# Optimization experiments

Hardware: AMD Instinct MI355X
Metric: run time of the kernel (lower is better)

## Reference

```python
import jax, jax.numpy as jnp
import numpy as np

N_NODES = 8192
EMBED = 64
N_NEURONS = [512, 256, 128]
ACTION_SIZE = 8
BATCH = 4096


def setup_inputs() -> dict:
    key = jax.random.key(0)
    ks = jax.random.split(key, 16)
    in_size = 2 * N_NODES + 2 * EMBED

    def u(k, shape, bound):
        return jax.random.uniform(k, shape, jnp.float32, -bound, bound)

    stdv1 = 1.0 / np.sqrt(N_NEURONS[0])
    stdv2 = 1.0 / np.sqrt(EMBED)
    return {
        "state": jax.random.uniform(ks[0], (N_NODES, N_NODES), jnp.float32),
        "start": jax.random.randint(ks[1], (BATCH,), 0, N_NODES),
        "end": jax.random.randint(ks[2], (BATCH,), 0, N_NODES),
        # GCN layer params
        "gw1": u(ks[3], (1, N_NEURONS[0]), stdv1),
        "gb1": u(ks[4], (N_NEURONS[0],), stdv1),
        "gw2": u(ks[5], (N_NEURONS[0], EMBED), stdv2),
        "gb2": u(ks[6], (EMBED,), stdv2),
        # dense head params (xavier-ish)
        "fw1": u(ks[7], (in_size, N_NEURONS[0]), np.sqrt(6.0 / (in_size + N_NEURONS[0]))),
        "fb1": jnp.zeros((N_NEURONS[0],), jnp.float32),
        "fw2": u(ks[8], (N_NEURONS[0], N_NEURONS[1]), np.sqrt(6.0 / (N_NEURONS[0] + N_NEURONS[1]))),
        "fb2": jnp.zeros((N_NEURONS[1],), jnp.float32),
        "fw3": u(ks[9], (N_NEURONS[1], N_NEURONS[2]), np.sqrt(6.0 / (N_NEURONS[1] + N_NEURONS[2]))),
        "fb3": jnp.zeros((N_NEURONS[2],), jnp.float32),
        "fw4": u(ks[10], (N_NEURONS[2], ACTION_SIZE), np.sqrt(6.0 / (N_NEURONS[2] + ACTION_SIZE))),
        "fb4": jnp.zeros((ACTION_SIZE,), jnp.float32),
    }


def reference(state, start, end, gw1, gb1, gw2, gb2,
              fw1, fb1, fw2, fb2, fw3, fb3, fw4, fb4):
    # x = diag(state) as [N, 1] node features
    x = jnp.diagonal(state)[:, None]
    # adj = state with zeroed diagonal, detached (no grad through adj)
    adj = jax.lax.stop_gradient(jnp.fill_diagonal(state, 0.0, inplace=False))
    # GCN layer 1: relu(adj @ (x @ W) + b); dropout is identity in eval mode
    h = jax.nn.relu(adj @ (x @ gw1) + gb1)              # [N, 512]
    # GCN layer 2
    h = jax.nn.relu(adj @ (h @ gw2) + gb2)              # [N, 64]
    h = jax.nn.log_softmax(h, axis=1)                   # [N, 64]
    # gather node features and embeddings for each (start, end) edge
    edge_features = jnp.concatenate(
        [state[start], state[end], h[start], h[end]], axis=1)  # [B, 2N+2E]
    y = jax.nn.relu(edge_features @ fw1 + fb1)
    y = jax.nn.relu(y @ fw2 + fb2)                      # d1 dropout: identity (eval)
    y = jax.nn.relu(y @ fw3 + fb3)
    action_q = jax.nn.relu(y @ fw4 + fb4)               # [B, action_size]
    return action_q
```

## Files before the change

### kernel.cpp

```cpp
#include <hip/hip_runtime.h>
#include <hip/hip_bf16.h>
#include <math.h>

#define NN 8192
#define EMB 64
#define H1D 512
#define NB 4096

typedef __bf16 bf16x8 __attribute__((ext_vector_type(8)));
typedef float f32x4 __attribute__((ext_vector_type(4)));
typedef unsigned short u16x8 __attribute__((ext_vector_type(8)));
typedef unsigned short u16x4 __attribute__((ext_vector_type(4)));

__device__ __forceinline__ unsigned short f2bf(float f) {
    return __bfloat16_as_ushort(__float2bfloat16(f));
}

__device__ __forceinline__ void gload16(const void* g, void* l) {
    __builtin_amdgcn_global_load_lds(
        (const __attribute__((address_space(1))) void*)g,
        (__attribute__((address_space(3))) void*)l, 16, 0, 0);
}

__global__ void k_diag(const float* __restrict__ state, float* __restrict__ diag) {
    int i = blockIdx.x * blockDim.x + threadIdx.x;
    if (i < NN) diag[i] = state[(size_t)i * NN + i];
}

__global__ __launch_bounds__(256) void k_convert(const float* __restrict__ state,
                                                 const float* __restrict__ diag,
                                                 unsigned short* __restrict__ stateb,
                                                 float* __restrict__ s) {
    int row = blockIdx.x;
    int tid = threadIdx.x;
    const float4* st4 = (const float4*)(state + (size_t)row * NN);
    const float4* dg4 = (const float4*)diag;
    unsigned short* drow = stateb + (size_t)row * NN;
    float acc = 0.f;
#pragma unroll
    for (int t = 0; t < 8; ++t) {
        int f = t * 256 + tid;
        float4 a = st4[f], d = dg4[f];
        acc += a.x * d.x + a.y * d.y + a.z * d.z + a.w * d.w;
        u16x4 o;
        o[0] = f2bf(a.x); o[1] = f2bf(a.y); o[2] = f2bf(a.z); o[3] = f2bf(a.w);
        *(u16x4*)&drow[f * 4] = o;
    }
#pragma unroll
    for (int m = 32; m >= 1; m >>= 1) acc += __shfl_xor(acc, m);
    __shared__ float red[4];
    if ((tid & 63) == 0) red[tid >> 6] = acc;
    __syncthreads();
    if (tid == 0) {
        float tot = red[0] + red[1] + red[2] + red[3];
        float d = diag[row];
        s[row] = tot - d * d;
    }
}

__global__ __launch_bounds__(256) void k_tr_fw1(const float* __restrict__ fw1,
                                                unsigned short* __restrict__ fw1t) {
    __shared__ float t[64][65];
    int kb = blockIdx.x * 64, nb = blockIdx.y * 64;
    int tid = threadIdx.x;
#pragma unroll
    for (int i = 0; i < 4; ++i) {
        int lin = i * 256 + tid;
        int r = lin >> 4, c4 = (lin & 15) << 2;
        float4 v = *(const float4*)&fw1[(size_t)(kb + r) * 512 + nb + c4];
        t[r][c4] = v.x; t[r][c4 + 1] = v.y; t[r][c4 + 2] = v.z; t[r][c4 + 3] = v.w;
    }
    __syncthreads();
#pragma unroll
    for (int i = 0; i < 4; ++i) {
        int lin = i * 256 + tid;
        int n = lin >> 4, k4 = (lin & 15) << 2;
        u16x4 o;
        o[0] = f2bf(t[k4 + 0][n]); o[1] = f2bf(t[k4 + 1][n]);
        o[2] = f2bf(t[k4 + 2][n]); o[3] = f2bf(t[k4 + 3][n]);
        *(u16x4*)&fw1t[(size_t)(nb + n) * 16512 + kb + k4] = o;
    }
}

__global__ __launch_bounds__(256) void k_tr_w(const float* __restrict__ W,
                                              unsigned short* __restrict__ Wt,
                                              int K, int N) {
    __shared__ float t[64][65];
    int kb = blockIdx.x * 64, nb = blockIdx.y * 64;
    int tid = threadIdx.x;
#pragma unroll
    for (int i = 0; i < 4; ++i) {
        int lin = i * 256 + tid;
        int r = lin >> 4, c4 = (lin & 15) << 2;
        float4 v = *(const float4*)&W[(size_t)(kb + r) * N + nb + c4];
        t[r][c4] = v.x; t[r][c4 + 1] = v.y; t[r][c4 + 2] = v.z; t[r][c4 + 3] = v.w;
    }
    __syncthreads();
#pragma unroll
    for (int i = 0; i < 4; ++i) {
        int lin = i * 256 + tid;
        int n = lin >> 4, k4 = (lin & 15) << 2;
        u16x4 o;
        o[0] = f2bf(t[k4 + 0][n]); o[1] = f2bf(t[k4 + 1][n]);
        o[2] = f2bf(t[k4 + 2][n]); o[3] = f2bf(t[k4 + 3][n]);
        *(u16x4*)&Wt[(size_t)(nb + n) * K + kb + k4] = o;
    }
}

__global__ __launch_bounds__(256) void k_tr_q(const float* __restrict__ q,
                                              unsigned short* __restrict__ qbT) {
    __shared__ float t[64][65];
    int kb = blockIdx.x * 64;
    int tid = threadIdx.x;
#pragma unroll
    for (int i = 0; i < 4; ++i) {
        int lin = i * 256 + tid;
        int r = lin >> 4, c4 = (lin & 15) << 2;
        float4 v = *(const float4*)&q[(size_t)(kb + r) * 64 + c4];
        t[r][c4] = v.x; t[r][c4 + 1] = v.y; t[r][c4 + 2] = v.z; t[r][c4 + 3] = v.w;
    }
    __syncthreads();
#pragma unroll
    for (int i = 0; i < 4; ++i) {
        int lin = i * 256 + tid;
        int c = lin >> 4, k4 = (lin & 15) << 2;
        u16x4 o;
        o[0] = f2bf(t[k4 + 0][c]); o[1] = f2bf(t[k4 + 1][c]);
        o[2] = f2bf(t[k4 + 2][c]); o[3] = f2bf(t[k4 + 3][c]);
        *(u16x4*)&qbT[(size_t)c * 8192 + kb + k4] = o;
    }
}

__global__ __launch_bounds__(256) void k_rowdot(const float* __restrict__ state,
                                                const float* __restrict__ diag,
                                                float* __restrict__ s) {
    int row = blockIdx.x;
    int tid = threadIdx.x;
    const float4* st4 = (const float4*)(state + (size_t)row * NN);
    const float4* dg4 = (const float4*)diag;
    float acc = 0.f;
#pragma unroll
    for (int t = 0; t < 8; ++t) {
        int f = t * 256 + tid;
        float4 a = st4[f], d = dg4[f];
        acc += a.x * d.x + a.y * d.y + a.z * d.z + a.w * d.w;
    }
#pragma unroll
    for (int m = 32; m >= 1; m >>= 1) acc += __shfl_xor(acc, m);
    __shared__ float red[4];
    if ((tid & 63) == 0) red[tid >> 6] = acc;
    __syncthreads();
    if (tid == 0) {
        float tot = red[0] + red[1] + red[2] + red[3];
        float d = diag[row];
        s[row] = tot - d * d;
    }
}

__global__ __launch_bounds__(256) void k_q(const float* __restrict__ s,
                                           const float* __restrict__ gw1,
                                           const float* __restrict__ gb1,
                                           const float* __restrict__ gw2,
                                           float* __restrict__ q) {
    __shared__ float sg1[H1D], sb1[H1D];
    int tid = threadIdx.x;
    for (int i = tid; i < H1D; i += 256) { sg1[i] = gw1[i]; sb1[i] = gb1[i]; }
    __syncthreads();
    int c = tid & 63;
    int row = blockIdx.x * 4 + (tid >> 6);
    float sv = s[row];
    float a0 = 0.f, a1 = 0.f, a2 = 0.f, a3 = 0.f;
    for (int j = 0; j < H1D; j += 4) {
        float h0 = fmaxf(fmaf(sv, sg1[j + 0], sb1[j + 0]), 0.f);
        float h1 = fmaxf(fmaf(sv, sg1[j + 1], sb1[j + 1]), 0.f);
        float h2 = fmaxf(fmaf(sv, sg1[j + 2], sb1[j + 2]), 0.f);
        float h3 = fmaxf(fmaf(sv, sg1[j + 3], sb1[j + 3]), 0.f);
        a0 = fmaf(h0, gw2[(j + 0) * EMB + c], a0);
        a1 = fmaf(h1, gw2[(j + 1) * EMB + c], a1);
        a2 = fmaf(h2, gw2[(j + 2) * EMB + c], a2);
        a3 = fmaf(h3, gw2[(j + 3) * EMB + c], a3);
    }
    q[row * EMB + c] = (a0 + a1) + (a2 + a3);
}


__global__ __launch_bounds__(256) void k_gcn2_mfma_b(const unsigned short* __restrict__ stateb,
                                                     const unsigned short* __restrict__ qbT,
                                                     float* __restrict__ partg) {
    __shared__ __align__(16) unsigned short Asm[2][64 * 64];
    __shared__ __align__(16) unsigned short Bsm[2][64 * 64];
    const int tid = threadIdx.x;
    const int l = tid & 63, wv = tid >> 6;
    const int rbase = blockIdx.x * 64;
    const int kbase0 = blockIdx.y * 1024;

    const unsigned short* aP[2]; const unsigned short* bP[2]; int lb[2];
#pragma unroll
    for (int i = 0; i < 2; ++i) {
        int slot = i * 256 + tid;
        int r = slot >> 3, cg = slot & 7;
        aP[i] = stateb + (size_t)(rbase + r) * NN + kbase0 + ((cg ^ (r & 7)) << 3);
        bP[i] = qbT + (size_t)r * 8192 + kbase0 + ((cg ^ (r & 7)) << 3);
        lb[i] = slot * 8;
    }

    f32x4 acc[4] = {};
    const int fr = l & 15, fq = l >> 4;

#pragma unroll
    for (int i = 0; i < 2; ++i) {
        gload16(aP[i], &Asm[0][lb[i]]);
        gload16(bP[i], &Bsm[0][lb[i]]);
    }
    __syncthreads();

    int buf = 0;
    for (int kt = 0; kt < 16; ++kt) {
        if (kt < 15) {
#pragma unroll
            for (int i = 0; i < 2; ++i) {
                gload16(aP[i] + (kt + 1) * 64, &Asm[buf ^ 1][lb[i]]);
                gload16(bP[i] + (kt + 1) * 64, &Bsm[buf ^ 1][lb[i]]);
            }
        }
#pragma unroll
        for (int kh = 0; kh < 2; ++kh) {
            int ch = kh * 4 + fq;
            int row = wv * 16 + fr;
            bf16x8 aF = *(const bf16x8*)&Asm[buf][row * 64 + ((ch ^ (row & 7)) << 3)];
            bf16x8 bF[4];
#pragma unroll
            for (int n = 0; n < 4; ++n) {
                int col = n * 16 + fr;
                bF[n] = *(const bf16x8*)&Bsm[buf][col * 64 + ((ch ^ (col & 7)) << 3)];
            }
#pragma unroll
            for (int n = 0; n < 4; ++n)
                acc[n] = __builtin_amdgcn_mfma_f32_16x16x32_bf16(aF, bF[n], acc[n], 0, 0, 0);
        }
        __syncthreads();
        buf ^= 1;
    }

    float* dst = partg + (size_t)blockIdx.y * (NN * EMB);
#pragma unroll
    for (int n = 0; n < 4; ++n) {
        int row0 = rbase + wv * 16 + fq * 4;
        int col = n * 16 + fr;
#pragma unroll
        for (int j = 0; j < 4; ++j)
            dst[(size_t)(row0 + j) * EMB + col] = acc[n][j];
    }
}

__global__ __launch_bounds__(256) void k_gcn2_combine_b(const float* __restrict__ partg,
                                                        const float* __restrict__ diag,
                                                        const float* __restrict__ q,
                                                        const float* __restrict__ gb2,
                                                        unsigned short* __restrict__ hb) {
    int tid = threadIdx.x;
    int c = tid & 63;
    int row = blockIdx.x * 4 + (tid >> 6);
    int idx = row * EMB + c;
    float v = gb2[c] - diag[row] * q[idx];
#pragma unroll
    for (int p = 0; p < 8; ++p) v += partg[(size_t)p * NN * EMB + idx];
    v = fmaxf(v, 0.f);
    float mx = v;
#pragma unroll
    for (int m = 32; m >= 1; m >>= 1) mx = fmaxf(mx, __shfl_xor(mx, m));
    float e = expf(v - mx);
    float sum = e;
#pragma unroll
    for (int m = 32; m >= 1; m >>= 1) sum += __shfl_xor(sum, m);
    hb[idx] = f2bf(v - mx - logf(sum));
}

__global__ __launch_bounds__(256) void k_head1_mfma_b(
    const unsigned short* __restrict__ stateb, const unsigned short* __restrict__ hb,
    const int* __restrict__ start, const int* __restrict__ end,
    const unsigned short* __restrict__ fw1t, float* __restrict__ parth) {
    __shared__ __align__(16) unsigned short Asm[128 * 64];
    __shared__ __align__(16) unsigned short Bsm[128 * 64];
    __shared__ int ridx[128];
    const int tid = threadIdx.x;
    const int l = tid & 63, wv = tid >> 6;
    const int rbase = blockIdx.x * 128, cbase = blockIdx.y * 128;
    const int ks = blockIdx.z, side = ks >> 1, half = ks & 1;
    if (tid < 128) ridx[tid] = (side ? end : start)[rbase + tid];
    __syncthreads();

    const unsigned short* aS[4]; const unsigned short* aH[4];
    const unsigned short* bP[4];
    unsigned short* aL[4]; unsigned short* bL[4];
#pragma unroll
    for (int i = 0; i < 4; ++i) {
        int slot = i * 256 + tid;
        int r = slot >> 3, cg = slot & 7;
        int swz = (cg ^ (r & 7)) << 3;
        int gi = ridx[r];
        aS[i] = stateb + (size_t)gi * NN + half * 4096 + swz;
        aH[i] = hb + gi * EMB + swz;
        bP[i] = fw1t + (size_t)(cbase + r) * 16512 + swz;
        aL[i] = &Asm[slot * 8];
        bL[i] = &Bsm[slot * 8];
    }
    const int kB0 = side * 8192 + half * 4096;
    const int kBtail = 16384 + side * 64;
    const int nsteps = 64 + half;

    f32x4 acc[4][4] = {};
    const int wm = wv >> 1, wn = wv & 1;
    const int fr = l & 15, fq = l >> 4;

    for (int kt = 0; kt < nsteps; ++kt) {
        if (kt < 64) {
#pragma unroll
            for (int i = 0; i < 4; ++i) {
                gload16(aS[i] + kt * 64, aL[i]);
                gload16(bP[i] + kB0 + kt * 64, bL[i]);
            }
        } else {
#pragma unroll
            for (int i = 0; i < 4; ++i) {
                gload16(aH[i], aL[i]);
                gload16(bP[i] + kBtail, bL[i]);
            }
        }
        __syncthreads();
#pragma unroll
        for (int kh = 0; kh < 2; ++kh) {
            int ch = kh * 4 + fq;
            bf16x8 aF[4], bF[4];
#pragma unroll
            for (int m = 0; m < 4; ++m) {
                int row = wm * 64 + m * 16 + fr;
                aF[m] = *(const bf16x8*)&Asm[row * 64 + ((ch ^ (row & 7)) << 3)];
            }
#pragma unroll
            for (int n = 0; n < 4; ++n) {
                int nl = wn * 64 + n * 16 + fr;
                bF[n] = *(const bf16x8*)&Bsm[nl * 64 + ((ch ^ (nl & 7)) << 3)];
            }
#pragma unroll
            for (int m = 0; m < 4; ++m)
#pragma unroll
                for (int n = 0; n < 4; ++n)
                    acc[m][n] = __builtin_amdgcn_mfma_f32_16x16x32_bf16(
                        aF[m], bF[n], acc[m][n], 0, 0, 0);
        }
        __syncthreads();
    }

    float* dst = parth + (size_t)ks * (NB * H1D);
#pragma unroll
    for (int m = 0; m < 4; ++m) {
        int row0 = rbase + wm * 64 + m * 16 + fq * 4;
#pragma unroll
        for (int n = 0; n < 4; ++n) {
            int col = cbase + wn * 64 + n * 16 + fr;
#pragma unroll
            for (int j = 0; j < 4; ++j)
                dst[(size_t)(row0 + j) * H1D + col] = acc[m][n][j];
        }
    }
}

__global__ void k_head1_fin4(const float* __restrict__ parth, const float* __restrict__ fb1,
                             unsigned short* __restrict__ y1b) {
    int i = blockIdx.x * blockDim.x + threadIdx.x;
    const size_t S = (size_t)NB * H1D;
    float4 a = *(const float4*)&parth[(size_t)i * 4];
    float4 b = *(const float4*)&parth[S + (size_t)i * 4];
    float4 c = *(const float4*)&parth[2 * S + (size_t)i * 4];
    float4 d = *(const float4*)&parth[3 * S + (size_t)i * 4];
    float4 bias = *(const float4*)&fb1[(i * 4) & 511];
    u16x4 o;
    o[0] = f2bf(fmaxf(a.x + b.x + c.x + d.x + bias.x, 0.f));
    o[1] = f2bf(fmaxf(a.y + b.y + c.y + d.y + bias.y, 0.f));
    o[2] = f2bf(fmaxf(a.z + b.z + c.z + d.z + bias.z, 0.f));
    o[3] = f2bf(fmaxf(a.w + b.w + c.w + d.w + bias.w, 0.f));
    *(u16x4*)&y1b[(size_t)i * 4] = o;
}

__global__ __launch_bounds__(256) void k_ff1(const unsigned short* __restrict__ A,
                                             const unsigned short* __restrict__ Wt,
                                             const float* __restrict__ bias,
                                             unsigned short* __restrict__ out) {
    __shared__ __align__(16) unsigned short Asm[128 * 64];
    __shared__ __align__(16) unsigned short Bsm[128 * 64];
    const int tid = threadIdx.x;
    const int l = tid & 63, wv = tid >> 6;
    const int rbase = blockIdx.x * 128, cbase = blockIdx.y * 128;

    const unsigned short* aP[4]; const unsigned short* bP[4];
    unsigned short* aL[4]; unsigned short* bL[4];
#pragma unroll
    for (int i = 0; i < 4; ++i) {
        int slot = i * 256 + tid;
        int r = slot >> 3, cg = slot & 7;
        int swz = (cg ^ (r & 7)) << 3;
        aP[i] = A + (size_t)(rbase + r) * 512 + swz;
        bP[i] = Wt + (size_t)(cbase + r) * 512 + swz;
        aL[i] = &Asm[slot * 8];
        bL[i] = &Bsm[slot * 8];
    }

    f32x4 acc[4][4] = {};
    const int wm = wv >> 1, wn = wv & 1;
    const int fr = l & 15, fq = l >> 4;

    for (int kt = 0; kt < 8; ++kt) {
#pragma unroll
        for (int i = 0; i < 4; ++i) {
            gload16(aP[i] + kt * 64, aL[i]);
            gload16(bP[i] + kt * 64, bL[i]);
        }
        __syncthreads();
#pragma unroll
        for (int kh = 0; kh < 2; ++kh) {
            int ch = kh * 4 + fq;
            bf16x8 aF[4], bF[4];
#pragma unroll
            for (int m = 0; m < 4; ++m) {
                int row = wm * 64 + m * 16 + fr;
                aF[m] = *(const bf16x8*)&Asm[row * 64 + ((ch ^ (row & 7)) << 3)];
            }
#pragma unroll
            for (int n = 0; n < 4; ++n) {
                int nl = wn * 64 + n * 16 + fr;
                bF[n] = *(const bf16x8*)&Bsm[nl * 64 + ((ch ^ (nl & 7)) << 3)];
            }
#pragma unroll
            for (int m = 0; m < 4; ++m)
#pragma unroll
                for (int n = 0; n < 4; ++n)
                    acc[m][n] = __builtin_amdgcn_mfma_f32_16x16x32_bf16(
                        aF[m], bF[n], acc[m][n], 0, 0, 0);
        }
        __syncthreads();
    }

#pragma unroll
    for (int m = 0; m < 4; ++m) {
        int row0 = rbase + wm * 64 + m * 16 + fq * 4;
#pragma unroll
        for (int n = 0; n < 4; ++n) {
            int col = cbase + wn * 64 + n * 16 + fr;
            float bv = bias[col];
#pragma unroll
            for (int j = 0; j < 4; ++j)
                out[(size_t)(row0 + j) * 256 + col] = f2bf(fmaxf(acc[m][n][j] + bv, 0.f));
        }
    }
}

__global__ __launch_bounds__(256) void k_ff2(const unsigned short* __restrict__ A,
                                             const unsigned short* __restrict__ Wt,
                                             const float* __restrict__ bias,
                                             float* __restrict__ out) {
    __shared__ __align__(16) unsigned short Asm[128 * 64];
    __shared__ __align__(16) unsigned short Bsm[128 * 64];
    const int tid = threadIdx.x;
    const int l = tid & 63, wv = tid >> 6;
    const int rbase = blockIdx.x * 128, cbase = 0;

    const unsigned short* aP[4]; const unsigned short* bP[4];
    unsigned short* aL[4]; unsigned short* bL[4];
#pragma unroll
    for (int i = 0; i < 4; ++i) {
        int slot = i * 256 + tid;
        int r = slot >> 3, cg = slot & 7;
        int swz = (cg ^ (r & 7)) << 3;
        aP[i] = A + (size_t)(rbase + r) * 256 + swz;
        bP[i] = Wt + (size_t)(cbase + r) * 256 + swz;
        aL[i] = &Asm[slot * 8];
        bL[i] = &Bsm[slot * 8];
    }

    f32x4 acc[4][4] = {};
    const int wm = wv >> 1, wn = wv & 1;
    const int fr = l & 15, fq = l >> 4;

    for (int kt = 0; kt < 4; ++kt) {
#pragma unroll
        for (int i = 0; i < 4; ++i) {
            gload16(aP[i] + kt * 64, aL[i]);
            gload16(bP[i] + kt * 64, bL[i]);
        }
        __syncthreads();
#pragma unroll
        for (int kh = 0; kh < 2; ++kh) {
            int ch = kh * 4 + fq;
            bf16x8 aF[4], bF[4];
#pragma unroll
            for (int m = 0; m < 4; ++m) {
                int row = wm * 64 + m * 16 + fr;
                aF[m] = *(const bf16x8*)&Asm[row * 64 + ((ch ^ (row & 7)) << 3)];
            }
#pragma unroll
            for (int n = 0; n < 4; ++n) {
                int nl = wn * 64 + n * 16 + fr;
                bF[n] = *(const bf16x8*)&Bsm[nl * 64 + ((ch ^ (nl & 7)) << 3)];
            }
#pragma unroll
            for (int m = 0; m < 4; ++m)
#pragma unroll
                for (int n = 0; n < 4; ++n)
                    acc[m][n] = __builtin_amdgcn_mfma_f32_16x16x32_bf16(
                        aF[m], bF[n], acc[m][n], 0, 0, 0);
        }
        __syncthreads();
    }

#pragma unroll
    for (int m = 0; m < 4; ++m) {
        int row0 = rbase + wm * 64 + m * 16 + fq * 4;
#pragma unroll
        for (int n = 0; n < 4; ++n) {
            int col = cbase + wn * 64 + n * 16 + fr;
            float bv = bias[col];
#pragma unroll
            for (int j = 0; j < 4; ++j)
                out[(size_t)(row0 + j) * 128 + col] = fmaxf(acc[m][n][j] + bv, 0.f);
        }
    }
}


__global__ __launch_bounds__(256) void k_gcn2_mfma(const float* __restrict__ state,
                                                   const unsigned short* __restrict__ qbT,
                                                   float* __restrict__ partg) {
    __shared__ __align__(16) unsigned short Asm[2][64 * 64];
    __shared__ __align__(16) unsigned short Bsm[2][64 * 64];
    const int tid = threadIdx.x;
    const int l = tid & 63, wv = tid >> 6;
    const int rbase = blockIdx.x * 64;
    const int kbase0 = blockIdx.y * 1024;

    const float* aptr[2]; int awr[2];
#pragma unroll
    for (int i = 0; i < 2; ++i) {
        int slot = i * 256 + tid;
        int r = slot >> 3, cg = slot & 7;
        aptr[i] = state + (size_t)(rbase + r) * NN + kbase0 + cg * 8;
        awr[i] = r * 64 + ((cg ^ (r & 7)) << 3);
    }
    const unsigned short* bptr[2]; int bbase[2];
#pragma unroll
    for (int i = 0; i < 2; ++i) {
        int c = i * 32 + wv * 8 + (l >> 3);
        int cg = l & 7;
        bptr[i] = qbT + (size_t)c * 8192 + kbase0 + ((cg ^ (c & 7)) << 3);
        bbase[i] = i * 2048 + wv * 512;
    }

    f32x4 acc[4] = {};
    const int fr = l & 15, fq = l >> 4;
    float4 va[2][2];

#pragma unroll
    for (int i = 0; i < 2; ++i) {
        va[i][0] = *(const float4*)aptr[i];
        va[i][1] = *(const float4*)(aptr[i] + 4);
    }
#pragma unroll
    for (int i = 0; i < 2; ++i) {
        u16x8 o;
        o[0] = f2bf(va[i][0].x); o[1] = f2bf(va[i][0].y); o[2] = f2bf(va[i][0].z); o[3] = f2bf(va[i][0].w);
        o[4] = f2bf(va[i][1].x); o[5] = f2bf(va[i][1].y); o[6] = f2bf(va[i][1].z); o[7] = f2bf(va[i][1].w);
        *(u16x8*)&Asm[0][awr[i]] = o;
        gload16(bptr[i], &Bsm[0][bbase[i]]);
    }
    __syncthreads();

    int buf = 0;
    for (int kt = 0; kt < 16; ++kt) {
        if (kt < 15) {
#pragma unroll
            for (int i = 0; i < 2; ++i) {
                gload16(bptr[i] + (kt + 1) * 64, &Bsm[buf ^ 1][bbase[i]]);
                va[i][0] = *(const float4*)(aptr[i] + (kt + 1) * 64);
                va[i][1] = *(const float4*)(aptr[i] + (kt + 1) * 64 + 4);
            }
        }
#pragma unroll
        for (int kh = 0; kh < 2; ++kh) {
            int ch = kh * 4 + fq;
            int row = wv * 16 + fr;
            bf16x8 aF = *(const bf16x8*)&Asm[buf][row * 64 + ((ch ^ (row & 7)) << 3)];
            bf16x8 bF[4];
#pragma unroll
            for (int n = 0; n < 4; ++n) {
                int col = n * 16 + fr;
                bF[n] = *(const bf16x8*)&Bsm[buf][col * 64 + ((ch ^ (col & 7)) << 3)];
            }
#pragma unroll
            for (int n = 0; n < 4; ++n)
                acc[n] = __builtin_amdgcn_mfma_f32_16x16x32_bf16(aF, bF[n], acc[n], 0, 0, 0);
        }
        if (kt < 15) {
#pragma unroll
            for (int i = 0; i < 2; ++i) {
                u16x8 o;
                o[0] = f2bf(va[i][0].x); o[1] = f2bf(va[i][0].y); o[2] = f2bf(va[i][0].z); o[3] = f2bf(va[i][0].w);
                o[4] = f2bf(va[i][1].x); o[5] = f2bf(va[i][1].y); o[6] = f2bf(va[i][1].z); o[7] = f2bf(va[i][1].w);
                *(u16x8*)&Asm[buf ^ 1][awr[i]] = o;
            }
        }
        __syncthreads();
        buf ^= 1;
    }

    float* dst = partg + (size_t)blockIdx.y * (NN * EMB);
#pragma unroll
    for (int n = 0; n < 4; ++n) {
        int row0 = rbase + wv * 16 + fq * 4;
        int col = n * 16 + fr;
#pragma unroll
        for (int j = 0; j < 4; ++j)
            dst[(size_t)(row0 + j) * EMB + col] = acc[n][j];
    }
}

__global__ __launch_bounds__(256) void k_gcn2_combine(const float* __restrict__ partg,
                                                      const float* __restrict__ diag,
                                                      const float* __restrict__ q,
                                                      const float* __restrict__ gb2,
                                                      float* __restrict__ h) {
    int tid = threadIdx.x;
    int c = tid & 63;
    int row = blockIdx.x * 4 + (tid >> 6);
    int idx = row * EMB + c;
    float v = gb2[c] - diag[row] * q[idx];
#pragma unroll
    for (int p = 0; p < 8; ++p) v += partg[(size_t)p * NN * EMB + idx];
    v = fmaxf(v, 0.f);
    float mx = v;
#pragma unroll
    for (int m = 32; m >= 1; m >>= 1) mx = fmaxf(mx, __shfl_xor(mx, m));
    float e = expf(v - mx);
    float sum = e;
#pragma unroll
    for (int m = 32; m >= 1; m >>= 1) sum += __shfl_xor(sum, m);
    h[idx] = v - mx - logf(sum);
}

__global__ __launch_bounds__(256) void k_head1_mfma(
    const float* __restrict__ state, const float* __restrict__ h,
    const int* __restrict__ start, const int* __restrict__ end,
    const unsigned short* __restrict__ fw1t, float* __restrict__ part) {
    __shared__ __align__(16) unsigned short Asm[2][64 * 64];
    __shared__ __align__(16) unsigned short Bsm[2][128 * 64];
    __shared__ int ridx[64];
    const int tid = threadIdx.x;
    const int l = tid & 63, wv = tid >> 6;
    const int rbase = blockIdx.x * 64, cbase = blockIdx.y * 128;
    const int ks = blockIdx.z;
    if (tid < 64) ridx[tid] = (ks ? end : start)[rbase + tid];
    __syncthreads();

    const float* aptr[2]; const float* hptr[2]; int awr[2];
#pragma unroll
    for (int i = 0; i < 2; ++i) {
        int slot = i * 256 + tid;
        int r = slot >> 3, cg = slot & 7;
        int gi = ridx[r];
        aptr[i] = state + (size_t)gi * NN + cg * 8;
        hptr[i] = h + gi * EMB + cg * 8;
        awr[i] = r * 64 + ((cg ^ (r & 7)) << 3);
    }
    const unsigned short* bptr[4]; int bbase[4];
#pragma unroll
    for (int i = 0; i < 4; ++i) {
        int n = i * 32 + wv * 8 + (l >> 3);
        int cg = l & 7;
        bptr[i] = fw1t + (size_t)(cbase + n) * 16512 + ((cg ^ (n & 7)) << 3);
        bbase[i] = i * 2048 + wv * 512;
    }

    f32x4 acc[2][4] = {};
    const int wm = wv >> 1, wn = wv & 1;
    const int fr = l & 15, fq = l >> 4;
    float4 va[2][2];

#pragma unroll
    for (int i = 0; i < 2; ++i) {
        va[i][0] = *(const float4*)aptr[i];
        va[i][1] = *(const float4*)(aptr[i] + 4);
    }
#pragma unroll
    for (int i = 0; i < 2; ++i) {
        u16x8 o;
        o[0] = f2bf(va[i][0].x); o[1] = f2bf(va[i][0].y); o[2] = f2bf(va[i][0].z); o[3] = f2bf(va[i][0].w);
        o[4] = f2bf(va[i][1].x); o[5] = f2bf(va[i][1].y); o[6] = f2bf(va[i][1].z); o[7] = f2bf(va[i][1].w);
        *(u16x8*)&Asm[0][awr[i]] = o;
    }
#pragma unroll
    for (int i = 0; i < 4; ++i) gload16(bptr[i] + ks * 8192, &Bsm[0][bbase[i]]);
    __syncthreads();

    int buf = 0;
    for (int kt = 0; kt < 129; ++kt) {
        if (kt < 128) {
            int nxt = kt + 1;
            int kB = (nxt < 128) ? (ks * 8192 + nxt * 64) : (16384 + ks * 64);
#pragma unroll
            for (int i = 0; i < 4; ++i) gload16(bptr[i] + kB, &Bsm[buf ^ 1][bbase[i]]);
#pragma unroll
            for (int i = 0; i < 2; ++i) {
                const float* src = (nxt < 128) ? (aptr[i] + nxt * 64) : hptr[i];
                va[i][0] = *(const float4*)src;
                va[i][1] = *(const float4*)(src + 4);
            }
        }
#pragma unroll
        for (int kh = 0; kh < 2; ++kh) {
            int ch = kh * 4 + fq;
            bf16x8 aF[2], bF[4];
#pragma unroll
            for (int m = 0; m < 2; ++m) {
                int row = wm * 32 + m * 16 + fr;
                aF[m] = *(const bf16x8*)&Asm[buf][row * 64 + ((ch ^ (row & 7)) << 3)];
            }
#pragma unroll
            for (int n = 0; n < 4; ++n) {
                int nl = wn * 64 + n * 16 + fr;
                bF[n] = *(const bf16x8*)&Bsm[buf][nl * 64 + ((ch ^ (nl & 7)) << 3)];
            }
#pragma unroll
            for (int m = 0; m < 2; ++m)
#pragma unroll
                for (int n = 0; n < 4; ++n)
                    acc[m][n] = __builtin_amdgcn_mfma_f32_16x16x32_bf16(
                        aF[m], bF[n], acc[m][n], 0, 0, 0);
        }
        if (kt < 128) {
#pragma unroll
            for (int i = 0; i < 2; ++i) {
                u16x8 o;
                o[0] = f2bf(va[i][0].x); o[1] = f2bf(va[i][0].y); o[2] = f2bf(va[i][0].z); o[3] = f2bf(va[i][0].w);
                o[4] = f2bf(va[i][1].x); o[5] = f2bf(va[i][1].y); o[6] = f2bf(va[i][1].z); o[7] = f2bf(va[i][1].w);
                *(u16x8*)&Asm[buf ^ 1][awr[i]] = o;
            }
        }
        __syncthreads();
        buf ^= 1;
    }

    float* dst = part + (size_t)ks * (NB * H1D);
#pragma unroll
    for (int m = 0; m < 2; ++m) {
        int row0 = rbase + wm * 32 + m * 16 + fq * 4;
#pragma unroll
        for (int n = 0; n < 4; ++n) {
            int col = cbase + wn * 64 + n * 16 + fr;
#pragma unroll
            for (int j = 0; j < 4; ++j)
                dst[(size_t)(row0 + j) * H1D + col] = acc[m][n][j];
        }
    }
}

__global__ void k_head1_fin(const float* __restrict__ part, const float* __restrict__ fb1,
                            float* __restrict__ y1) {
    int i = blockIdx.x * blockDim.x + threadIdx.x;
    float4 a = *(const float4*)&part[(size_t)i * 4];
    float4 b = *(const float4*)&part[(size_t)NB * H1D + (size_t)i * 4];
    float4 bias = *(const float4*)&fb1[(i * 4) & 511];
    float4 o;
    o.x = fmaxf(a.x + b.x + bias.x, 0.f);
    o.y = fmaxf(a.y + b.y + bias.y, 0.f);
    o.z = fmaxf(a.z + b.z + bias.z, 0.f);
    o.w = fmaxf(a.w + b.w + bias.w, 0.f);
    *(float4*)&y1[(size_t)i * 4] = o;
}

#define GEMM_INNER(AsM, BsM)                                          \
    _Pragma("unroll")                                                 \
    for (int k4 = 0; k4 < 64; k4 += 4) {                              \
        float av[4][4], bv[4][4];                                     \
        _Pragma("unroll")                                             \
        for (int i = 0; i < 4; ++i)                                   \
            *(float4*)av[i] = *(const float4*)&AsM[4 * row_t + i][k4];\
        _Pragma("unroll")                                             \
        for (int t = 0; t < 4; ++t)                                   \
            *(float4*)bv[t] = *(const float4*)&BsM[k4 + t][4 * col_t];\
        _Pragma("unroll")                                             \
        for (int i = 0; i < 4; ++i) {                                 \
            _Pragma("unroll")                                         \
            for (int t = 0; t < 4; ++t) {                             \
                _Pragma("unroll")                                     \
                for (int j = 0; j < 4; ++j)                           \
                    acc[i][j] = fmaf(av[i][t], bv[t][j], acc[i][j]);  \
            }                                                         \
        }                                                             \
    }

__global__ __launch_bounds__(256) void k_gemm_relu(const float* __restrict__ A,
                                                   const float* __restrict__ W,
                                                   const float* __restrict__ bias,
                                                   float* __restrict__ C,
                                                   int M, int N, int K) {
    __shared__ __align__(16) float As[64][68];
    __shared__ __align__(16) float Bs[64][68];
    int tid = threadIdx.x;
    int rbase = blockIdx.x * 64;
    int cbase = blockIdx.y * 64;
    int row_t = tid >> 4, col_t = tid & 15;
    float acc[4][4] = {};
    for (int kt = 0; kt < K / 64; ++kt) {
        int kbase = kt * 64;
#pragma unroll
        for (int l = 0; l < 4; ++l) {
            int lin = l * 256 + tid;
            int r = lin >> 4, k4 = (lin & 15) << 2;
            float4 v = *(const float4*)&A[(size_t)(rbase + r) * K + kbase + k4];
            As[r][k4 + 0] = v.x; As[r][k4 + 1] = v.y; As[r][k4 + 2] = v.z; As[r][k4 + 3] = v.w;
            float4 w = *(const float4*)&W[(size_t)(kbase + r) * N + cbase + k4];
            Bs[r][k4 + 0] = w.x; Bs[r][k4 + 1] = w.y; Bs[r][k4 + 2] = w.z; Bs[r][k4 + 3] = w.w;
        }
        __syncthreads();
        GEMM_INNER(As, Bs)
        __syncthreads();
    }
#pragma unroll
    for (int i = 0; i < 4; ++i) {
        int row = rbase + 4 * row_t + i;
        int col = cbase + 4 * col_t;
        float4 v;
        v.x = fmaxf(acc[i][0] + bias[col + 0], 0.f);
        v.y = fmaxf(acc[i][1] + bias[col + 1], 0.f);
        v.z = fmaxf(acc[i][2] + bias[col + 2], 0.f);
        v.w = fmaxf(acc[i][3] + bias[col + 3], 0.f);
        *(float4*)&C[(size_t)row * N + col] = v;
    }
}

__global__ void k_head4(const float* __restrict__ y3, const float* __restrict__ fw4,
                        const float* __restrict__ fb4, float* __restrict__ out) {
    int tid = blockIdx.x * blockDim.x + threadIdx.x;
    int b = tid >> 3, j = tid & 7;
    float acc = fb4[j];
    for (int k = 0; k < 128; ++k)
        acc = fmaf(y3[b * 128 + k], fw4[k * 8 + j], acc);
    out[tid] = fmaxf(acc, 0.f);
}

extern "C" void kernel_launch(void* const* d_in, const int* in_sizes, int n_in,
                              void* d_out, int out_size, void* d_ws, size_t ws_size,
                              hipStream_t stream) {
    const float* state = (const float*)d_in[0];
    const int* start   = (const int*)d_in[1];
    const int* end     = (const int*)d_in[2];
    const float* gw1   = (const float*)d_in[3];
    const float* gb1   = (const float*)d_in[4];
    const float* gw2   = (const float*)d_in[5];
    const float* gb2   = (const float*)d_in[6];
    const float* fw1   = (const float*)d_in[7];
    const float* fb1   = (const float*)d_in[8];
    const float* fw2   = (const float*)d_in[9];
    const float* fb2   = (const float*)d_in[10];
    const float* fw3   = (const float*)d_in[11];
    const float* fb3   = (const float*)d_in[12];
    const float* fw4   = (const float*)d_in[13];
    const float* fb4   = (const float*)d_in[14];
    float* out = (float*)d_out;
    float* ws = (float*)d_ws;

    const size_t NEED_BIG = 53084160ull * 4ull;
    const size_t NEED_FB  = 9748480ull * 4ull;

    if (ws_size >= NEED_BIG) {
        float* diag = ws;
        float* s    = ws + 8192;
        float* q    = ws + 16384;
        unsigned short* qbT = (unsigned short*)(ws + 540672);
        unsigned short* hb  = (unsigned short*)(ws + 802816);
        float* partg = ws + 1064960;
        unsigned short* fw1t = (unsigned short*)(ws + 5259264);
        unsigned short* stateb = (unsigned short*)(ws + 9486336);
        float* parth = ws + 43040768;
        unsigned short* fw2t = (unsigned short*)(ws + 51429376);
        unsigned short* fw3t = (unsigned short*)(ws + 51494912);
        unsigned short* y1b  = (unsigned short*)(ws + 51511296);
        unsigned short* y2b  = (unsigned short*)(ws + 52559872);
        float* y3   = ws + 7356416;

        k_diag<<<32, 256, 0, stream>>>(state, diag);
        k_convert<<<8192, 256, 0, stream>>>(state, diag, stateb, s);
        k_tr_fw1<<<dim3(258, 8), 256, 0, stream>>>(fw1, fw1t);
        k_tr_w<<<dim3(8, 4), 256, 0, stream>>>(fw2, fw2t, 512, 256);
        k_tr_w<<<dim3(4, 2), 256, 0, stream>>>(fw3, fw3t, 256, 128);
        k_q<<<2048, 256, 0, stream>>>(s, gw1, gb1, gw2, q);
        k_tr_q<<<128, 256, 0, stream>>>(q, qbT);
        k_gcn2_mfma_b<<<dim3(128, 8), 256, 0, stream>>>(stateb, qbT, partg);
        k_gcn2_combine_b<<<2048, 256, 0, stream>>>(partg, diag, q, gb2, hb);
        k_head1_mfma_b<<<dim3(32, 4, 4), 256, 0, stream>>>(stateb, hb, start, end, fw1t, parth);
        k_head1_fin4<<<2048, 256, 0, stream>>>(parth, fb1, y1b);
        k_ff1<<<dim3(32, 2), 256, 0, stream>>>(y1b, fw2t, fb2, y2b);
        k_ff2<<<dim3(32, 1), 256, 0, stream>>>(y2b, fw3t, fb3, y3);
        k_head4<<<128, 256, 0, stream>>>(y3, fw4, fb4, out);
        return;
    }

    if (ws_size < NEED_FB) return;

    float* diag = ws;
    float* s    = ws + 8192;
    float* q    = ws + 16384;
    unsigned short* qbT = (unsigned short*)(ws + 540672);
    float* h    = ws + 802816;
    float* partg = ws + 1327104;
    unsigned short* fw1t = (unsigned short*)(ws + 5521408);
    float* parth = ws + 1327104;
    float* y1   = ws + 5521408;
    float* y2   = ws + 16384;
    float* y3   = ws + 7618560;

    k_diag<<<32, 256, 0, stream>>>(state, diag);
    k_tr_fw1<<<dim3(258, 8), 256, 0, stream>>>(fw1, fw1t);
    k_rowdot<<<8192, 256, 0, stream>>>(state, diag, s);
    k_q<<<2048, 256, 0, stream>>>(s, gw1, gb1, gw2, q);
    k_tr_q<<<128, 256, 0, stream>>>(q, qbT);
    k_gcn2_mfma<<<dim3(128, 8), 256, 0, stream>>>(state, qbT, partg);
    k_gcn2_combine<<<2048, 256, 0, stream>>>(partg, diag, q, gb2, h);
    k_head1_mfma<<<dim3(64, 4, 2), 256, 0, stream>>>(state, h, start, end, fw1t, parth);
    k_head1_fin<<<2048, 256, 0, stream>>>(parth, fb1, y1);
    k_gemm_relu<<<dim3(64, 4), 256, 0, stream>>>(y1, fw2, fb2, y2, NB, 256, 512);
    k_gemm_relu<<<dim3(64, 2), 256, 0, stream>>>(y2, fw3, fb3, y3, NB, 128, 256);
    k_head4<<<128, 256, 0, stream>>>(y3, fw4, fb4, out);
}
```

Measured before the change: 278.0 us.

## Double-buffer head1 GEMM and use partial vmcnt waits with setprio in both MFMA kernels

The head1 GEMM, which previously loaded a single LDS buffer and then waited on it, now double-buffers with a prefetch of the next K tile while the current one is computed. Both the gcn2 and head1 kernels replace __syncthreads with explicit s_waitcnt vmcnt(N) plus raw s_barrier. This lets the newest prefetch stay in flight, and s_setprio raises wave priority around the MFMA bursts. The head1 kernel's LDS use doubles to 64KB, which may reduce occupancy. Hand-counted vmcnt values are fragile if the compiler emits other vector memory ops.

Result: no change. 276.2 us (median of 2 runs) (-0.7%).

```diff
diff --git a/kernel.cpp b/kernel.cpp
--- a/kernel.cpp
+++ b/kernel.cpp
@@ -184,6 +184,23 @@
 }
 
 
+#define GCN2_MFMA(BUF)                                                              \
+    _Pragma("unroll")                                                               \
+    for (int kh = 0; kh < 2; ++kh) {                                                \
+        int ch = kh * 4 + fq;                                                       \
+        int row = wv * 16 + fr;                                                     \
+        bf16x8 aF = *(const bf16x8*)&Asm[BUF][row * 64 + ((ch ^ (row & 7)) << 3)];  \
+        bf16x8 bF[4];                                                               \
+        _Pragma("unroll")                                                           \
+        for (int n = 0; n < 4; ++n) {                                               \
+            int col = n * 16 + fr;                                                  \
+            bF[n] = *(const bf16x8*)&Bsm[BUF][col * 64 + ((ch ^ (col & 7)) << 3)];  \
+        }                                                                           \
+        _Pragma("unroll")                                                           \
+        for (int n = 0; n < 4; ++n)                                                 \
+            acc[n] = __builtin_amdgcn_mfma_f32_16x16x32_bf16(aF, bF[n], acc[n], 0, 0, 0); \
+    }
+
 __global__ __launch_bounds__(256) void k_gcn2_mfma_b(const unsigned short* __restrict__ stateb,
                                                      const unsigned short* __restrict__ qbT,
                                                      float* __restrict__ partg) {
@@ -212,35 +229,28 @@
         gload16(aP[i], &Asm[0][lb[i]]);
         gload16(bP[i], &Bsm[0][lb[i]]);
     }
-    __syncthreads();
 
     int buf = 0;
-    for (int kt = 0; kt < 16; ++kt) {
-        if (kt < 15) {
-#pragma unroll
-            for (int i = 0; i < 2; ++i) {
-                gload16(aP[i] + (kt + 1) * 64, &Asm[buf ^ 1][lb[i]]);
-                gload16(bP[i] + (kt + 1) * 64, &Bsm[buf ^ 1][lb[i]]);
-            }
-        }
-#pragma unroll
-        for (int kh = 0; kh < 2; ++kh) {
-            int ch = kh * 4 + fq;
-            int row = wv * 16 + fr;
-            bf16x8 aF = *(const bf16x8*)&Asm[buf][row * 64 + ((ch ^ (row & 7)) << 3)];
-            bf16x8 bF[4];
-#pragma unroll
-            for (int n = 0; n < 4; ++n) {
-                int col = n * 16 + fr;
-                bF[n] = *(const bf16x8*)&Bsm[buf][col * 64 + ((ch ^ (col & 7)) << 3)];
-            }
-#pragma unroll
-            for (int n = 0; n < 4; ++n)
-                acc[n] = __builtin_amdgcn_mfma_f32_16x16x32_bf16(aF, bF[n], acc[n], 0, 0, 0);
-        }
-        __syncthreads();
+    for (int kt = 0; kt < 15; ++kt) {
+#pragma unroll
+        for (int i = 0; i < 2; ++i) {
+            gload16(aP[i] + (kt + 1) * 64, &Asm[buf ^ 1][lb[i]]);
+            gload16(bP[i] + (kt + 1) * 64, &Bsm[buf ^ 1][lb[i]]);
+        }
+        asm volatile("s_waitcnt vmcnt(4)" ::: "memory");
+        __builtin_amdgcn_s_barrier();
+        __builtin_amdgcn_sched_barrier(0);
+        __builtin_amdgcn_s_setprio(1);
+        GCN2_MFMA(buf)
+        __builtin_amdgcn_s_setprio(0);
+        __builtin_amdgcn_sched_barrier(0);
+        __builtin_amdgcn_s_barrier();
         buf ^= 1;
     }
+    asm volatile("s_waitcnt vmcnt(0)" ::: "memory");
+    __builtin_amdgcn_s_barrier();
+    __builtin_amdgcn_sched_barrier(0);
+    GCN2_MFMA(buf)
 
     float* dst = partg + (size_t)blockIdx.y * (NN * EMB);
 #pragma unroll
@@ -276,12 +286,35 @@
     hb[idx] = f2bf(v - mx - logf(sum));
 }
 
+#define HEAD1_MFMA(BUF)                                                             \
+    _Pragma("unroll")                                                               \
+    for (int kh = 0; kh < 2; ++kh) {                                                \
+        int ch = kh * 4 + fq;                                                       \
+        bf16x8 aF[4], bF[4];                                                        \
+        _Pragma("unroll")                                                           \
+        for (int m = 0; m < 4; ++m) {                                               \
+            int row = wm * 64 + m * 16 + fr;                                        \
+            aF[m] = *(const bf16x8*)&Asm[BUF][row * 64 + ((ch ^ (row & 7)) << 3)];  \
+        }                                                                           \
+        _Pragma("unroll")                                                           \
+        for (int n = 0; n < 4; ++n) {                                               \
+            int nl = wn * 64 + n * 16 + fr;                                         \
+            bF[n] = *(const bf16x8*)&Bsm[BUF][nl * 64 + ((ch ^ (nl & 7)) << 3)];    \
+        }                                                                           \
+        _Pragma("unroll")                                                           \
+        for (int m = 0; m < 4; ++m)                                                 \
+            _Pragma("unroll")                                                       \
+            for (int n = 0; n < 4; ++n)                                             \
+                acc[m][n] = __builtin_amdgcn_mfma_f32_16x16x32_bf16(                \
+                    aF[m], bF[n], acc[m][n], 0, 0, 0);                              \
+    }
+
 __global__ __launch_bounds__(256) void k_head1_mfma_b(
     const unsigned short* __restrict__ stateb, const unsigned short* __restrict__ hb,
     const int* __restrict__ start, const int* __restrict__ end,
     const unsigned short* __restrict__ fw1t, float* __restrict__ parth) {
-    __shared__ __align__(16) unsigned short Asm[128 * 64];
-    __shared__ __align__(16) unsigned short Bsm[128 * 64];
+    __shared__ __align__(16) unsigned short Asm[2][128 * 64];
+    __shared__ __align__(16) unsigned short Bsm[2][128 * 64];
     __shared__ int ridx[128];
     const int tid = threadIdx.x;
     const int l = tid & 63, wv = tid >> 6;
@@ -292,7 +325,7 @@
 
     const unsigned short* aS[4]; const unsigned short* aH[4];
     const unsigned short* bP[4];
-    unsigned short* aL[4]; unsigned short* bL[4];
+    int aLo[4], bLo[4];
 #pragma unroll
     for (int i = 0; i < 4; ++i) {
         int slot = i * 256 + tid;
@@ -302,8 +335,8 @@
         aS[i] = stateb + (size_t)gi * NN + half * 4096 + swz;
         aH[i] = hb + gi * EMB + swz;
         bP[i] = fw1t + (size_t)(cbase + r) * 16512 + swz;
-        aL[i] = &Asm[slot * 8];
-        bL[i] = &Bsm[slot * 8];
+        aLo[i] = slot * 8;
+        bLo[i] = slot * 8;
     }
     const int kB0 = side * 8192 + half * 4096;
     const int kBtail = 16384 + side * 64;
@@ -313,44 +346,42 @@
     const int wm = wv >> 1, wn = wv & 1;
     const int fr = l & 15, fq = l >> 4;
 
-    for (int kt = 0; kt < nsteps; ++kt) {
-        if (kt < 64) {
+#pragma unroll
+    for (int i = 0; i < 4; ++i) {
+        gload16(aS[i], &Asm[0][aLo[i]]);
+        gload16(bP[i] + kB0, &Bsm[0][bLo[i]]);
+    }
+
+    int buf = 0;
+    for (int kt = 0; kt < nsteps - 1; ++kt) {
+        int nxt = kt + 1;
+        if (nxt < 64) {
 #pragma unroll
             for (int i = 0; i < 4; ++i) {
-                gload16(aS[i] + kt * 64, aL[i]);
-                gload16(bP[i] + kB0 + kt * 64, bL[i]);
+                gload16(aS[i] + nxt * 64, &Asm[buf ^ 1][aLo[i]]);
+                gload16(bP[i] + kB0 + nxt * 64, &Bsm[buf ^ 1][bLo[i]]);
             }
         } else {
 #pragma unroll
             for (int i = 0; i < 4; ++i) {
-                gload16(aH[i], aL[i]);
-                gload16(bP[i] + kBtail, bL[i]);
-            }
-        }
-        __syncthreads();
-#pragma unroll
-        for (int kh = 0; kh < 2; ++kh) {
-            int ch = kh * 4 + fq;
-            bf16x8 aF[4], bF[4];
-#pragma unroll
-            for (int m = 0; m < 4; ++m) {
-                int row = wm * 64 + m * 16 + fr;
-                aF[m] = *(const bf16x8*)&Asm[row * 64 + ((ch ^ (row & 7)) << 3)];
-            }
-#pragma unroll
-            for (int n = 0; n < 4; ++n) {
-                int nl = wn * 64 + n * 16 + fr;
-                bF[n] = *(const bf16x8*)&Bsm[nl * 64 + ((ch ^ (nl & 7)) << 3)];
-            }
-#pragma unroll
-            for (int m = 0; m < 4; ++m)
-#pragma unroll
-                for (int n = 0; n < 4; ++n)
-                    acc[m][n] = __builtin_amdgcn_mfma_f32_16x16x32_bf16(
-                        aF[m], bF[n], acc[m][n], 0, 0, 0);
-        }
-        __syncthreads();
-    }
+                gload16(aH[i], &Asm[buf ^ 1][aLo[i]]);
+                gload16(bP[i] + kBtail, &Bsm[buf ^ 1][bLo[i]]);
+            }
+        }
+        asm volatile("s_waitcnt vmcnt(8)" ::: "memory");
+        __builtin_amdgcn_s_barrier();
+        __builtin_amdgcn_sched_barrier(0);
+        __builtin_amdgcn_s_setprio(1);
+        HEAD1_MFMA(buf)
+        __builtin_amdgcn_s_setprio(0);
+        __builtin_amdgcn_sched_barrier(0);
+        __builtin_amdgcn_s_barrier();
+        buf ^= 1;
+    }
+    asm volatile("s_waitcnt vmcnt(0)" ::: "memory");
+    __builtin_amdgcn_s_barrier();
+    __builtin_amdgcn_sched_barrier(0);
+    HEAD1_MFMA(buf)
 
     float* dst = parth + (size_t)ks * (NB * H1D);
 #pragma unroll
```
